# Kernel optimization log

Measured on AMD Instinct MI355X. Metric: run time of the kernel, lower is better.

Reference implementation:

```python
import jax, jax.numpy as jnp
import numpy as np

NS, NV = 32, 8                      # scalar / vector multiplicities
N_NODES, N_EDGES, N_EF = 10000, 100000, 64
W1, W2, W3, W4 = NS*NS, NV*NV, NS*NV, NV*NS   # path weight sizes
WNUM = W1 + W2 + W3 + W4            # 1600
D_NODE = NS + 3*NV                  # 56

def mish(x):
    return x * jnp.tanh(jax.nn.softplus(x))

def setup_inputs() -> dict:
    key = jax.random.key(0)
    ks = jax.random.split(key, 8)
    return dict(
        node_attr=jax.random.normal(ks[0], (N_NODES, D_NODE), jnp.float32),
        edge_index=jax.random.randint(ks[1], (2, N_EDGES), 0, N_NODES),
        edge_attr=jax.random.normal(ks[2], (N_EDGES, N_EF), jnp.float32),
        edge_sh=jax.random.normal(ks[3], (N_EDGES, 4), jnp.float32),
        fc1_w=jax.random.normal(ks[4], (N_EF, N_EF), jnp.float32) / np.sqrt(N_EF),
        fc1_b=jnp.zeros((N_EF,), jnp.float32),
        fc2_w=jax.random.normal(ks[5], (N_EF, WNUM), jnp.float32) / np.sqrt(N_EF),
        fc2_b=jnp.zeros((WNUM,), jnp.float32),
        bn_gamma_s=jnp.ones((NS,), jnp.float32),
        bn_beta_s=jnp.zeros((NS,), jnp.float32),
        bn_gamma_v=jnp.ones((NV,), jnp.float32),
    )

def reference(node_attr, edge_index, edge_attr, edge_sh,
              fc1_w, fc1_b, fc2_w, fc2_b,
              bn_gamma_s, bn_beta_s, bn_gamma_v):
    edge_src, edge_dst = edge_index[0], edge_index[1]
    # edge-conditioned TP weights: Linear -> Mish -> Linear
    w = mish(edge_attr @ fc1_w + fc1_b) @ fc2_w + fc2_b            # [E, WNUM]
    w1 = w[:, :W1].reshape(-1, NS, NS)           # 0e x 0e -> 0e
    w2 = w[:, W1:W1+W2].reshape(-1, NV, NV)      # 1o x 0e -> 1o
    w3 = w[:, W1+W2:W1+W2+W3].reshape(-1, NS, NV)  # 0e x 1o -> 1o
    w4 = w[:, W1+W2+W3:].reshape(-1, NV, NS)     # 1o x 1o -> 0e
    # gather destination node features
    x = node_attr[edge_dst]
    s = x[:, :NS]                                # [E,NS]
    v = x[:, NS:].reshape(-1, NV, 3)             # [E,NV,3]
    sh0 = edge_sh[:, 0]                          # [E]
    sh1 = edge_sh[:, 1:4]                        # [E,3]
    # path normalization: 1/sqrt(total fan-in per output irrep) = 1/sqrt(NS+NV)
    a = 1.0 / np.sqrt(float(NS + NV))
    dot = jnp.einsum('euc,ec->eu', v, sh1) / np.sqrt(3.0)  # CG(1,1,0)
    out_s = a * (jnp.einsum('eu,euw->ew', s * sh0[:, None], w1)
               + jnp.einsum('eu,euw->ew', dot, w4))          # [E,NS]
    out_v = a * (jnp.einsum('euc,euw->ewc', v * sh0[:, None, None], w2)
               + jnp.einsum('eu,ec,euw->ewc', s, sh1, w3))   # [E,NV,3]
    tp = jnp.concatenate([out_s, out_v.reshape(-1, 3*NV)], axis=-1)  # [E,D_NODE]
    # scatter-mean over edge_src
    summ = jax.ops.segment_sum(tp, edge_src, num_segments=N_NODES)
    cnt = jax.ops.segment_sum(jnp.ones((N_EDGES,), tp.dtype), edge_src, num_segments=N_NODES)
    out = summ / jnp.maximum(cnt, 1.0)[:, None]
    # residual (in/out irreps equal -> pad is a no-op)
    out = out + node_attr
    # e3nn-style BatchNorm (training batch stats), eps=1e-4, component norm
    eps = 1e-4
    os = out[:, :NS]
    ov = out[:, NS:].reshape(-1, NV, 3)
    mu = os.mean(axis=0)
    osc = os - mu
    var = (osc * osc).mean(axis=0)
    os_n = osc * jax.lax.rsqrt(var + eps) * bn_gamma_s + bn_beta_s
    vn = (ov * ov).mean(axis=-1).mean(axis=0)                 # [NV]
    ov_n = ov * (jax.lax.rsqrt(vn + eps) * bn_gamma_v)[None, :, None]
    return jnp.concatenate([os_n, ov_n.reshape(-1, 3*NV)], axis=-1)
```

## Files before the change

### kernel.cpp

```cpp
#include <hip/hip_runtime.h>
#include <stdint.h>

#define NNODES 10000
#define NEDGES 100000
#define DNODE 56
#define JTOT 1600
#define EBLK 782
#define TBLK 400

typedef __attribute__((ext_vector_type(8))) short short8;
typedef __attribute__((ext_vector_type(4))) float floatx4;

__device__ __forceinline__ unsigned short f2bf(float f) {
  unsigned u = __float_as_uint(f);
  u = u + 0x7fffu + ((u >> 16) & 1u);
  return (unsigned short)(u >> 16);
}
__device__ __forceinline__ float bf2f(unsigned short u) {
  return __uint_as_float(((unsigned)u) << 16);
}

__device__ __forceinline__ float mishf(float x) {
  float e = __expf(x);
  float z = 1.f + e; z = z * z;
  float t = (z - 1.f) / (z + 1.f);
  t = (x > 40.f) ? 1.f : t;
  return x * t;
}

__device__ __forceinline__ void async_ld16(void* lds, const void* gp) {
  __builtin_amdgcn_global_load_lds(
      (const __attribute__((address_space(1))) unsigned int*)gp,
      (__attribute__((address_space(3))) unsigned int*)lds, 16, 0, 0);
}

__global__ __launch_bounds__(256, 4) void k_hidtr(const float* __restrict__ ea,
                                                  const float* __restrict__ fc1w,
                                                  const float* __restrict__ fc1b,
                                                  const float* __restrict__ fc2w,
                                                  const int* __restrict__ eidx,
                                                  int* __restrict__ cntn,
                                                  unsigned short* __restrict__ hb,
                                                  unsigned short* __restrict__ G) {
  const int bid = blockIdx.x, tid = threadIdx.x;
  if (bid >= EBLK) {
    int idx = (bid - EBLK) * 256 + tid;
    if (idx < 64 * JTOT) {
      int jt = idx >> 10, r = idx & 1023;
      int c = r >> 6, w = r & 63;
      int slot = w >> 3, s = w & 7;
      int g = slot ^ (c & 7);
      int k = g * 8 + s;
      int j = jt * 16 + c;
      G[idx] = f2bf(fc2w[k * JTOT + j]);
    }
    return;
  }
  __shared__ unsigned short T[64 * 72];
  __shared__ unsigned short E[128 * 72];
  __shared__ float b1s[64];
  const int e0 = bid * 128;
  if (tid < 128) {
    int e = e0 + tid;
    if (e < NEDGES) atomicAdd(&cntn[eidx[e]], 1);
  }
  if (tid < 64) b1s[tid] = fc1b[tid];
  #pragma unroll
  for (int it = 0; it < 4; it++) {
    int q = tid + 256 * it;
    int k = q >> 4, j4 = (q & 15) * 4;
    float4 v = *(const float4*)(fc1w + (size_t)q * 4);
    T[(j4+0)*72 + k] = f2bf(v.x);
    T[(j4+1)*72 + k] = f2bf(v.y);
    T[(j4+2)*72 + k] = f2bf(v.z);
    T[(j4+3)*72 + k] = f2bf(v.w);
  }
  #pragma unroll
  for (int it = 0; it < 8; it++) {
    int q = tid + 256 * it;
    int e = q >> 4, k4 = (q & 15) * 4;
    int ge = e0 + e;
    float4 v = (ge < NEDGES) ? *(const float4*)(ea + (size_t)ge * 64 + k4)
                             : make_float4(0.f, 0.f, 0.f, 0.f);
    ushort4 p;
    p.x = f2bf(v.x); p.y = f2bf(v.y); p.z = f2bf(v.z); p.w = f2bf(v.w);
    *(ushort4*)(&E[e*72 + k4]) = p;
  }
  __syncthreads();

  const int wave = tid >> 6, lane = tid & 63, col = lane & 15, rg = lane >> 4;
  short8 bf[2][2];
  #pragma unroll
  for (int nt = 0; nt < 2; nt++) {
    int er = wave*32 + nt*16 + col;
    bf[nt][0] = *(const short8*)(&E[er*72 + rg*8]);
    bf[nt][1] = *(const short8*)(&E[er*72 + 32 + rg*8]);
  }
  floatx4 acc[4][2];
  #pragma unroll
  for (int jt = 0; jt < 4; jt++) {
    int j = jt*16 + col;
    short8 a0 = *(const short8*)(&T[j*72 + rg*8]);
    short8 a1 = *(const short8*)(&T[j*72 + 32 + rg*8]);
    float4 bb = *(const float4*)(&b1s[jt*16 + rg*4]);
    #pragma unroll
    for (int nt = 0; nt < 2; nt++) {
      floatx4 c = {bb.x, bb.y, bb.z, bb.w};
      c = __builtin_amdgcn_mfma_f32_16x16x32_bf16(a0, bf[nt][0], c, 0, 0, 0);
      c = __builtin_amdgcn_mfma_f32_16x16x32_bf16(a1, bf[nt][1], c, 0, 0, 0);
      acc[jt][nt] = c;
    }
  }
  #pragma unroll
  for (int jt = 0; jt < 4; jt++)
    #pragma unroll
    for (int nt = 0; nt < 2; nt++) {
      ushort4 p;
      p.x = f2bf(mishf(acc[jt][nt][0]));
      p.y = f2bf(mishf(acc[jt][nt][1]));
      p.z = f2bf(mishf(acc[jt][nt][2]));
      p.w = f2bf(mishf(acc[jt][nt][3]));
      *(ushort4*)(&E[(wave*32 + nt*16 + col)*72 + jt*16 + rg*4]) = p;
    }
  #pragma unroll
  for (int it = 0; it < 4; it++) {
    int g = it*64 + lane;
    int r = g >> 3, c = g & 7;
    int ge = e0 + wave*32 + r;
    if (ge < NEDGES) {
      short8 v = *(const short8*)(&E[(wave*32 + r)*72 + c*8]);
      *(short8*)(hb + (size_t)ge*64 + c*8) = v;
    }
  }
}

__global__ __launch_bounds__(1024) void k_scan(const int* __restrict__ cntn,
                                               int* __restrict__ offs,
                                               int* __restrict__ cursor) {
  __shared__ int ts[1024];
  int t = threadIdx.x;
  int base = t * 10;
  int loc[10]; int s = 0;
  #pragma unroll
  for (int i = 0; i < 10; i++) {
    int idx = base + i;
    int v = (idx < NNODES) ? cntn[idx] : 0;
    loc[i] = s; s += v;
  }
  ts[t] = s;
  __syncthreads();
  for (int off = 1; off < 1024; off <<= 1) {
    int v = (t >= off) ? ts[t - off] : 0;
    __syncthreads();
    ts[t] += v;
    __syncthreads();
  }
  int excl = (t == 0) ? 0 : ts[t - 1];
  #pragma unroll
  for (int i = 0; i < 10; i++) {
    int idx = base + i;
    if (idx < NNODES) { int o = excl + loc[i]; offs[idx] = o; cursor[idx] = o; }
  }
  if (t == 1023) offs[NNODES] = ts[1023];
}

__global__ __launch_bounds__(256, 4) void k_tp(
    const unsigned short* __restrict__ hb,
    const unsigned short* __restrict__ G,
    const float* __restrict__ fc2b,
    const int* __restrict__ eidx,
    const float* __restrict__ node_attr,
    const float* __restrict__ edge_sh,
    int* __restrict__ cursor,
    float* __restrict__ tp) {
  __shared__ short Gs[2][4 * 1024];
  __shared__ unsigned short wls[4][64 * 32];
  __shared__ float b2s[JTOT];
  __shared__ int pos_s[4][32];
  const int tid = threadIdx.x;
  const int wave = tid >> 6, lane = tid & 63;
  for (int i = tid; i < JTOT; i += 256) b2s[i] = fc2b[i];

  const int e0w = blockIdx.x * 128 + wave * 32;
  unsigned short* Wt = &wls[wave][0];
  {
    int el = lane & 31, hh = lane >> 5;
    int e = e0w + el;
    bool valid = e < NEDGES;
    int dst = valid ? eidx[NEDGES + e] : 0;
    const float* na = node_attr + (size_t)dst * DNODE;
    if (hh == 0) {
      pos_s[wave][el] = valid ? atomicAdd(&cursor[eidx[e]], 1) : 0;
      #pragma unroll
      for (int u = 0; u < 32; u += 4) {
        float4 v = valid ? *(const float4*)(na + u) : make_float4(0.f,0.f,0.f,0.f);
        Wt[(u+0)*32 + el] = f2bf(v.x);
        Wt[(u+1)*32 + el] = f2bf(v.y);
        Wt[(u+2)*32 + el] = f2bf(v.z);
        Wt[(u+3)*32 + el] = f2bf(v.w);
      }
    } else {
      float4 sh = valid ? *(const float4*)(edge_sh + 4*(size_t)e) : make_float4(0.f,0.f,0.f,0.f);
      const float rs3 = 0.57735026918962576f;
      #pragma unroll
      for (int u = 0; u < 8; u++) {
        float v0 = valid ? na[32 + u*3 + 0] : 0.f;
        float v1 = valid ? na[32 + u*3 + 1] : 0.f;
        float v2 = valid ? na[32 + u*3 + 2] : 0.f;
        Wt[(32 + u*3 + 0)*32 + el] = f2bf(v0);
        Wt[(32 + u*3 + 1)*32 + el] = f2bf(v1);
        Wt[(32 + u*3 + 2)*32 + el] = f2bf(v2);
        Wt[(56 + u)*32 + el] = f2bf((v0*sh.y + v1*sh.z + v2*sh.w) * rs3);
      }
    }
  }

  const int col = lane & 15, rg = lane >> 4, rgh = rg >> 1;
  const int g0 = (rg ^ (col & 7)) * 8;
  const int g1 = ((rg + 4) ^ (col & 7)) * 8;
  float sh0c[2], sh1c[2][3];
  bool vld[2];
  short8 bfrag[2][2];
  const short8 zfrag = {0,0,0,0,0,0,0,0};
  #pragma unroll
  for (int nt = 0; nt < 2; nt++) {
    int e = e0w + nt*16 + col;
    bool v = e < NEDGES; vld[nt] = v;
    if (v) {
      float4 sh = *(const float4*)(edge_sh + 4*(size_t)e);
      sh0c[nt] = sh.x; sh1c[nt][0] = sh.y; sh1c[nt][1] = sh.z; sh1c[nt][2] = sh.w;
      const unsigned short* hp = hb + (size_t)e * 64;
      bfrag[nt][0] = *(const short8*)(hp + rg*8);
      bfrag[nt][1] = *(const short8*)(hp + 32 + rg*8);
    } else {
      sh0c[nt] = 0.f; sh1c[nt][0] = sh1c[nt][1] = sh1c[nt][2] = 0.f;
      bfrag[nt][0] = zfrag; bfrag[nt][1] = zfrag;
    }
  }

  float sacc[2][8], vacc[2][12];
  #pragma unroll
  for (int nt = 0; nt < 2; nt++) {
    #pragma unroll
    for (int i = 0; i < 8; i++) sacc[nt][i] = 0.f;
    #pragma unroll
    for (int i = 0; i < 12; i++) vacc[nt][i] = 0.f;
  }

  auto stage = [&](int ch, int b) {
    const unsigned short* gsrc = G + (size_t)ch * 4096 + tid * 8;
    #pragma unroll
    for (int i = 0; i < 2; i++)
      async_ld16(&Gs[b][(i*256 + wave*64) * 8], gsrc + i*256*8);
  };

  const int cc0 = blockIdx.x % 25;
  stage(cc0, 0);
  __syncthreads();

  int buf = 0;
  #pragma unroll 1
  for (int cc = 0; cc < 25; cc++) {
    int c = cc0 + cc; if (c >= 25) c -= 25;
    if (cc < 24) { int cn = c + 1; if (cn >= 25) cn = 0; stage(cn, buf ^ 1); }
    #pragma unroll
    for (int t = 0; t < 4; t++) {
      const int jt = c * 4 + t;
      const short* gb = &Gs[buf][t * 1024];
      short8 x0 = *(const short8*)(gb + col*64 + g0);
      short8 x1 = *(const short8*)(gb + col*64 + g1);
      float4 bb = *(const float4*)&b2s[jt*16 + rg*4];
      floatx4 acc[2];
      #pragma unroll
      for (int nt = 0; nt < 2; nt++) {
        floatx4 a = {bb.x, bb.y, bb.z, bb.w};
        a = __builtin_amdgcn_mfma_f32_16x16x32_bf16(x0, bfrag[nt][0], a, 0, 0, 0);
        a = __builtin_amdgcn_mfma_f32_16x16x32_bf16(x1, bfrag[nt][1], a, 0, 0, 0);
        acc[nt] = a;
      }
      if (jt < 64) {
        const int u = jt >> 1, p = jt & 1;
        #pragma unroll
        for (int nt = 0; nt < 2; nt++) {
          float cf = bf2f(Wt[u*32 + nt*16 + col]) * sh0c[nt];
          #pragma unroll
          for (int r = 0; r < 4; r++)
            sacc[nt][p*4+r] = fmaf(cf, acc[nt][r], sacc[nt][p*4+r]);
        }
      } else if (jt < 68) {
        const int u = (jt - 64)*2 + rgh;
        #pragma unroll
        for (int nt = 0; nt < 2; nt++) {
          #pragma unroll
          for (int q = 0; q < 3; q++) {
            float cf = bf2f(Wt[(32 + u*3 + q)*32 + nt*16 + col]) * sh0c[nt];
            #pragma unroll
            for (int r = 0; r < 4; r++)
              vacc[nt][q*4+r] = fmaf(cf, acc[nt][r], vacc[nt][q*4+r]);
          }
        }
      } else if (jt < 84) {
        const int u = (jt - 68)*2 + rgh;
        #pragma unroll
        for (int nt = 0; nt < 2; nt++) {
          float sv = bf2f(Wt[u*32 + nt*16 + col]);
          #pragma unroll
          for (int q = 0; q < 3; q++) {
            float cf = sv * sh1c[nt][q];
            #pragma unroll
            for (int r = 0; r < 4; r++)
              vacc[nt][q*4+r] = fmaf(cf, acc[nt][r], vacc[nt][q*4+r]);
          }
        }
      } else {
        const int u = (jt - 84) >> 1, p = jt & 1;
        #pragma unroll
        for (int nt = 0; nt < 2; nt++) {
          float cf = bf2f(Wt[(56 + u)*32 + nt*16 + col]);
          #pragma unroll
          for (int r = 0; r < 4; r++)
            sacc[nt][p*4+r] = fmaf(cf, acc[nt][r], sacc[nt][p*4+r]);
        }
      }
    }
    buf ^= 1;
    __syncthreads();
  }

  const float ascale = 0.15811388300841897f;
  #pragma unroll
  for (int nt = 0; nt < 2; nt++) {
    int el = nt*16 + col;
    float* rowp = tp + (size_t)pos_s[wave][el] * DNODE;
    if (vld[nt]) {
      #pragma unroll
      for (int p = 0; p < 2; p++) {
        float4 v = make_float4(ascale*sacc[nt][p*4+0], ascale*sacc[nt][p*4+1],
                               ascale*sacc[nt][p*4+2], ascale*sacc[nt][p*4+3]);
        *(float4*)(rowp + p*16 + rg*4) = v;
      }
    }
    float vtot[12];
    #pragma unroll
    for (int k = 0; k < 12; k++)
      vtot[k] = (vacc[nt][k] + __shfl_xor(vacc[nt][k], 32)) * ascale;
    if (rg < 2 && vld[nt]) {
      float tmp[12];
      #pragma unroll
      for (int q = 0; q < 3; q++)
        #pragma unroll
        for (int r = 0; r < 4; r++) tmp[r*3 + q] = vtot[q*4 + r];
      #pragma unroll
      for (int j = 0; j < 3; j++)
        *(float4*)(rowp + 32 + (rg & 1)*12 + j*4) = *(float4*)&tmp[j*4];
    }
  }
}

__global__ __launch_bounds__(256) void k_gather(const float* __restrict__ tp,
                                                const int* __restrict__ offs,
                                                const float* __restrict__ node_attr,
                                                float* __restrict__ pre,
                                                float* __restrict__ pstat) {
  __shared__ float redS[4*64], redQ[4*64];
  int t = threadIdx.x, wave = t >> 6, lane = t & 63;
  int gw = blockIdx.x * 4 + wave;
  const int W = 640 * 4;
  int off = (lane < DNODE) ? lane : 0;
  float ssum = 0.f, ssq = 0.f;
  for (int n = gw; n < NNODES; n += W) {
    int beg = offs[n], end = offs[n+1];
    float acc = 0.f;
    int i = beg;
    for (; i + 4 <= end; i += 4) {
      float v0 = tp[(size_t)(i+0)*DNODE + off];
      float v1 = tp[(size_t)(i+1)*DNODE + off];
      float v2 = tp[(size_t)(i+2)*DNODE + off];
      float v3 = tp[(size_t)(i+3)*DNODE + off];
      acc += (v0 + v1) + (v2 + v3);
    }
    for (; i < end; i++) acc += tp[(size_t)i*DNODE + off];
    int c = end - beg; if (c < 1) c = 1;
    float m = acc / (float)c + node_attr[(size_t)n*DNODE + off];
    if (lane < DNODE) { pre[(size_t)n*DNODE + lane] = m; ssum += m; ssq += m*m; }
  }
  redS[wave*64 + lane] = ssum;
  redQ[wave*64 + lane] = ssq;
  __syncthreads();
  if (wave == 0 && lane < DNODE) {
    float a = redS[lane] + redS[64+lane] + redS[128+lane] + redS[192+lane];
    float b = redQ[lane] + redQ[64+lane] + redQ[128+lane] + redQ[192+lane];
    pstat[(size_t)blockIdx.x*112 + lane] = a;
    pstat[(size_t)blockIdx.x*112 + 56 + lane] = b;
  }
}

__global__ __launch_bounds__(256) void k_stats(const float* __restrict__ pstat,
                                               float* __restrict__ stats) {
  int f = blockIdx.x * 4 + (threadIdx.x >> 6);
  int lane = threadIdx.x & 63;
  float v = 0.f;
  for (int b = lane; b < 640; b += 64) v += pstat[(size_t)b*112 + f];
  #pragma unroll
  for (int o = 32; o; o >>= 1) v += __shfl_xor(v, o);
  if (lane == 0) stats[f] = v;
}

__global__ __launch_bounds__(256) void k_norm(const float* __restrict__ pre,
                                              const float* __restrict__ stats,
                                              const float* __restrict__ gs,
                                              const float* __restrict__ bs,
                                              const float* __restrict__ gv,
                                              float* __restrict__ out) {
  int idx = blockIdx.x * 256 + threadIdx.x;
  if (idx >= NNODES * DNODE) return;
  int n = idx / DNODE;
  int d = idx - n * DNODE;
  float val = pre[idx];
  const float invN = 1.f / (float)NNODES;
  float res;
  if (d < 32) {
    float mu = stats[d] * invN;
    float var = stats[56 + d] * invN - mu * mu;
    res = (val - mu) * rsqrtf(var + 1e-4f) * gs[d] + bs[d];
  } else {
    int wi = (d - 32) / 3;
    float vn = (stats[56 + 32 + wi*3] + stats[56 + 32 + wi*3 + 1] +
                stats[56 + 32 + wi*3 + 2]) * (invN / 3.f);
    res = val * rsqrtf(vn + 1e-4f) * gv[wi];
  }
  out[idx] = res;
}

extern "C" void kernel_launch(void* const* d_in, const int* in_sizes, int n_in,
                              void* d_out, int out_size, void* d_ws, size_t ws_size,
                              hipStream_t stream) {
  const float* node_attr = (const float*)d_in[0];
  const int*   eidx      = (const int*)d_in[1];
  const float* edge_attr = (const float*)d_in[2];
  const float* edge_sh   = (const float*)d_in[3];
  const float* fc1w      = (const float*)d_in[4];
  const float* fc1b      = (const float*)d_in[5];
  const float* fc2w      = (const float*)d_in[6];
  const float* fc2b      = (const float*)d_in[7];
  const float* gs        = (const float*)d_in[8];
  const float* bs        = (const float*)d_in[9];
  const float* gv        = (const float*)d_in[10];

  float* ws = (float*)d_ws;
  float* tp    = ws;
  float* pre   = ws + 5600000;
  float* stats = ws + 6160000;
  float* pstat = ws + 6160128;
  int*   cntn  = (int*)(ws + 6231808);
  int*   offs  = (int*)(ws + 6241808);
  int*   cursor= (int*)(ws + 6251816);
  unsigned short* G  = (unsigned short*)(ws + 6261816);
  unsigned short* hb = (unsigned short*)(ws + 6313016);

  hipMemsetAsync(cntn, 0, (size_t)10000 * 4, stream);
  k_hidtr<<<EBLK + TBLK, 256, 0, stream>>>(edge_attr, fc1w, fc1b, fc2w, eidx, cntn, hb, G);
  k_scan<<<1, 1024, 0, stream>>>(cntn, offs, cursor);
  k_tp<<<782, 256, 0, stream>>>(hb, G, fc2b, eidx, node_attr, edge_sh, cursor, tp);
  k_gather<<<640, 256, 0, stream>>>(tp, offs, node_attr, pre, pstat);
  k_stats<<<28, 256, 0, stream>>>(pstat, stats);
  k_norm<<<(NNODES * DNODE + 255) / 256, 256, 0, stream>>>(pre, stats, gs, bs, gv, (float*)d_out);
}
```

Before: 195.9 us.

## Switch TP GEMM to 32x32 MFMA tiles and fuse scan/stats into neighbors

The edge tensor-product kernel now uses 32x32x16 bf16 MFMA tiles, one 32-edge column per wave, with a re-laid-out fc2 weight matrix. This removes the cross-half shuffle reduction and lowers instruction count per output. Separately, the histogram and scan are done by one extra block inside the hidden-layer kernel, which eliminates the memset and the scan launch. The stats reduction is folded into the gather kernel through a last-block atomic counter, which removes another launch. The costs are a serial single-block histogram of 100k edges and higher LDS use, with occupancy dropped to 3 blocks.

After: 312.1 us. 59.3% more time.

```diff
diff --git a/kernel.cpp b/kernel.cpp
--- a/kernel.cpp
+++ b/kernel.cpp
@@ -9,7 +9,7 @@
 #define TBLK 400
 
 typedef __attribute__((ext_vector_type(8))) short short8;
-typedef __attribute__((ext_vector_type(4))) float floatx4;
+typedef __attribute__((ext_vector_type(16))) float floatx16;
 
 __device__ __forceinline__ unsigned short f2bf(float f) {
   unsigned u = __float_as_uint(f);
@@ -34,36 +34,69 @@
       (__attribute__((address_space(3))) unsigned int*)lds, 16, 0, 0);
 }
 
-__global__ __launch_bounds__(256, 4) void k_hidtr(const float* __restrict__ ea,
+__global__ __launch_bounds__(256, 3) void k_hidtr(const float* __restrict__ ea,
                                                   const float* __restrict__ fc1w,
                                                   const float* __restrict__ fc1b,
                                                   const float* __restrict__ fc2w,
                                                   const int* __restrict__ eidx,
-                                                  int* __restrict__ cntn,
+                                                  int* __restrict__ offs,
+                                                  int* __restrict__ cursor,
+                                                  int* __restrict__ gdone,
                                                   unsigned short* __restrict__ hb,
                                                   unsigned short* __restrict__ G) {
+  __shared__ int4 SM4[2576];
   const int bid = blockIdx.x, tid = threadIdx.x;
+
+  if (bid == EBLK + TBLK) {
+    int* hist = (int*)SM4;
+    int* ts   = hist + 10000;
+    for (int i = tid; i < NNODES; i += 256) hist[i] = 0;
+    if (tid == 0) gdone[0] = 0;
+    __syncthreads();
+    for (int i = tid; i < NEDGES; i += 256) atomicAdd(&hist[eidx[i]], 1);
+    __syncthreads();
+    int s = 0;
+    #pragma unroll 8
+    for (int i = 0; i < 40; i++) {
+      int idx = tid * 40 + i;
+      if (idx < NNODES) s += hist[idx];
+    }
+    ts[tid] = s;
+    __syncthreads();
+    for (int o = 1; o < 256; o <<= 1) {
+      int v = (tid >= o) ? ts[tid - o] : 0;
+      __syncthreads();
+      ts[tid] += v;
+      __syncthreads();
+    }
+    int run = (tid == 0) ? 0 : ts[tid - 1];
+    for (int i = 0; i < 40; i++) {
+      int idx = tid * 40 + i;
+      if (idx < NNODES) { int c = hist[idx]; offs[idx] = run; cursor[idx] = run; run += c; }
+    }
+    if (tid == 255) offs[NNODES] = ts[255];
+    return;
+  }
+
   if (bid >= EBLK) {
     int idx = (bid - EBLK) * 256 + tid;
     if (idx < 64 * JTOT) {
-      int jt = idx >> 10, r = idx & 1023;
-      int c = r >> 6, w = r & 63;
-      int slot = w >> 3, s = w & 7;
-      int g = slot ^ (c & 7);
-      int k = g * 8 + s;
-      int j = jt * 16 + c;
+      int jt = idx >> 11;
+      int r  = idx & 2047;
+      int s  = r >> 9;
+      int l  = (r >> 3) & 63;
+      int i  = r & 7;
+      int j  = jt * 32 + (l & 31);
+      int k  = s * 16 + (l >> 5) * 8 + i;
       G[idx] = f2bf(fc2w[k * JTOT + j]);
     }
     return;
   }
-  __shared__ unsigned short T[64 * 72];
-  __shared__ unsigned short E[128 * 72];
-  __shared__ float b1s[64];
+
+  unsigned short* T  = (unsigned short*)SM4;
+  unsigned short* E  = (unsigned short*)SM4 + 4608;
+  float* b1s = (float*)((char*)SM4 + 27648);
   const int e0 = bid * 128;
-  if (tid < 128) {
-    int e = e0 + tid;
-    if (e < NEDGES) atomicAdd(&cntn[eidx[e]], 1);
-  }
   if (tid < 64) b1s[tid] = fc1b[tid];
   #pragma unroll
   for (int it = 0; it < 4; it++) {
@@ -89,6 +122,7 @@
   __syncthreads();
 
   const int wave = tid >> 6, lane = tid & 63, col = lane & 15, rg = lane >> 4;
+  typedef __attribute__((ext_vector_type(4))) float floatx4;
   short8 bf[2][2];
   #pragma unroll
   for (int nt = 0; nt < 2; nt++) {
@@ -132,36 +166,6 @@
       *(short8*)(hb + (size_t)ge*64 + c*8) = v;
     }
   }
-}
-
-__global__ __launch_bounds__(1024) void k_scan(const int* __restrict__ cntn,
-                                               int* __restrict__ offs,
-                                               int* __restrict__ cursor) {
-  __shared__ int ts[1024];
-  int t = threadIdx.x;
-  int base = t * 10;
-  int loc[10]; int s = 0;
-  #pragma unroll
-  for (int i = 0; i < 10; i++) {
-    int idx = base + i;
-    int v = (idx < NNODES) ? cntn[idx] : 0;
-    loc[i] = s; s += v;
-  }
-  ts[t] = s;
-  __syncthreads();
-  for (int off = 1; off < 1024; off <<= 1) {
-    int v = (t >= off) ? ts[t - off] : 0;
-    __syncthreads();
-    ts[t] += v;
-    __syncthreads();
-  }
-  int excl = (t == 0) ? 0 : ts[t - 1];
-  #pragma unroll
-  for (int i = 0; i < 10; i++) {
-    int idx = base + i;
-    if (idx < NNODES) { int o = excl + loc[i]; offs[idx] = o; cursor[idx] = o; }
-  }
-  if (t == 1023) offs[NNODES] = ts[1023];
 }
 
 __global__ __launch_bounds__(256, 4) void k_tp(
@@ -173,8 +177,8 @@
     const float* __restrict__ edge_sh,
     int* __restrict__ cursor,
     float* __restrict__ tp) {
-  __shared__ short Gs[2][4 * 1024];
-  __shared__ unsigned short wls[4][64 * 32];
+  __shared__ short Gs[2][4096];
+  __shared__ unsigned short wls[4][2048];
   __shared__ float b2s[JTOT];
   __shared__ int pos_s[4][32];
   const int tid = threadIdx.x;
@@ -215,37 +219,30 @@
     }
   }
 
-  const int col = lane & 15, rg = lane >> 4, rgh = rg >> 1;
-  const int g0 = (rg ^ (col & 7)) * 8;
-  const int g1 = ((rg + 4) ^ (col & 7)) * 8;
-  float sh0c[2], sh1c[2][3];
-  bool vld[2];
-  short8 bfrag[2][2];
+  const int col = lane & 31, h = lane >> 5;
+  const int e = e0w + col;
+  const bool vld = e < NEDGES;
+  float sh0c, sh1c[3];
+  short8 bfr[4];
   const short8 zfrag = {0,0,0,0,0,0,0,0};
-  #pragma unroll
-  for (int nt = 0; nt < 2; nt++) {
-    int e = e0w + nt*16 + col;
-    bool v = e < NEDGES; vld[nt] = v;
-    if (v) {
-      float4 sh = *(const float4*)(edge_sh + 4*(size_t)e);
-      sh0c[nt] = sh.x; sh1c[nt][0] = sh.y; sh1c[nt][1] = sh.z; sh1c[nt][2] = sh.w;
-      const unsigned short* hp = hb + (size_t)e * 64;
-      bfrag[nt][0] = *(const short8*)(hp + rg*8);
-      bfrag[nt][1] = *(const short8*)(hp + 32 + rg*8);
-    } else {
-      sh0c[nt] = 0.f; sh1c[nt][0] = sh1c[nt][1] = sh1c[nt][2] = 0.f;
-      bfrag[nt][0] = zfrag; bfrag[nt][1] = zfrag;
-    }
-  }
-
-  float sacc[2][8], vacc[2][12];
-  #pragma unroll
-  for (int nt = 0; nt < 2; nt++) {
-    #pragma unroll
-    for (int i = 0; i < 8; i++) sacc[nt][i] = 0.f;
-    #pragma unroll
-    for (int i = 0; i < 12; i++) vacc[nt][i] = 0.f;
-  }
+  if (vld) {
+    float4 sh = *(const float4*)(edge_sh + 4*(size_t)e);
+    sh0c = sh.x; sh1c[0] = sh.y; sh1c[1] = sh.z; sh1c[2] = sh.w;
+    const unsigned short* hp = hb + (size_t)e * 64;
+    #pragma unroll
+    for (int s = 0; s < 4; s++)
+      bfr[s] = *(const short8*)(hp + s*16 + h*8);
+  } else {
+    sh0c = 0.f; sh1c[0] = sh1c[1] = sh1c[2] = 0.f;
+    #pragma unroll
+    for (int s = 0; s < 4; s++) bfr[s] = zfrag;
+  }
+
+  float sacc[16], vacc[12];
+  #pragma unroll
+  for (int i = 0; i < 16; i++) sacc[i] = 0.f;
+  #pragma unroll
+  for (int i = 0; i < 12; i++) vacc[i] = 0.f;
 
   auto stage = [&](int ch, int b) {
     const unsigned short* gsrc = G + (size_t)ch * 4096 + tid * 8;
@@ -254,106 +251,107 @@
       async_ld16(&Gs[b][(i*256 + wave*64) * 8], gsrc + i*256*8);
   };
 
+  int buf = 0;
+  auto gemm_tile = [&](int jt, int t) -> floatx16 {
+    const short* gb = &Gs[buf][t * 2048];
+    short8 a0 = *(const short8*)(gb + lane*8);
+    short8 a1 = *(const short8*)(gb + 512 + lane*8);
+    short8 a2 = *(const short8*)(gb + 1024 + lane*8);
+    short8 a3 = *(const short8*)(gb + 1536 + lane*8);
+    floatx16 C;
+    #pragma unroll
+    for (int q = 0; q < 4; q++) {
+      float4 b = *(const float4*)&b2s[jt*32 + 8*q + 4*h];
+      C[q*4+0] = b.x; C[q*4+1] = b.y; C[q*4+2] = b.z; C[q*4+3] = b.w;
+    }
+    C = __builtin_amdgcn_mfma_f32_32x32x16_bf16(a0, bfr[0], C, 0, 0, 0);
+    C = __builtin_amdgcn_mfma_f32_32x32x16_bf16(a1, bfr[1], C, 0, 0, 0);
+    C = __builtin_amdgcn_mfma_f32_32x32x16_bf16(a2, bfr[2], C, 0, 0, 0);
+    C = __builtin_amdgcn_mfma_f32_32x32x16_bf16(a3, bfr[3], C, 0, 0, 0);
+    return C;
+  };
+  auto apply_s = [&](const floatx16& C, float cf) {
+    #pragma unroll
+    for (int i = 0; i < 16; i++) sacc[i] = fmaf(cf, C[i], sacc[i]);
+  };
+  auto apply_w2 = [&](const floatx16& C, int ubase) {
+    #pragma unroll
+    for (int q = 0; q < 4; q++) {
+      const int u = ubase + q;
+      #pragma unroll
+      for (int c = 0; c < 3; c++) {
+        float cf = bf2f(Wt[(32 + u*3 + c)*32 + col]) * sh0c;
+        #pragma unroll
+        for (int r = 0; r < 4; r++)
+          vacc[c*4+r] = fmaf(cf, C[q*4+r], vacc[c*4+r]);
+      }
+    }
+  };
+  auto apply_w3 = [&](const floatx16& C, int ubase) {
+    #pragma unroll
+    for (int q = 0; q < 4; q++) {
+      float sv = bf2f(Wt[(ubase + q)*32 + col]);
+      #pragma unroll
+      for (int c = 0; c < 3; c++) {
+        float cf = sv * sh1c[c];
+        #pragma unroll
+        for (int r = 0; r < 4; r++)
+          vacc[c*4+r] = fmaf(cf, C[q*4+r], vacc[c*4+r]);
+      }
+    }
+  };
+
   const int cc0 = blockIdx.x % 25;
   stage(cc0, 0);
   __syncthreads();
 
-  int buf = 0;
   #pragma unroll 1
   for (int cc = 0; cc < 25; cc++) {
     int c = cc0 + cc; if (c >= 25) c -= 25;
     if (cc < 24) { int cn = c + 1; if (cn >= 25) cn = 0; stage(cn, buf ^ 1); }
-    #pragma unroll
-    for (int t = 0; t < 4; t++) {
-      const int jt = c * 4 + t;
-      const short* gb = &Gs[buf][t * 1024];
-      short8 x0 = *(const short8*)(gb + col*64 + g0);
-      short8 x1 = *(const short8*)(gb + col*64 + g1);
-      float4 bb = *(const float4*)&b2s[jt*16 + rg*4];
-      floatx4 acc[2];
-      #pragma unroll
-      for (int nt = 0; nt < 2; nt++) {
-        floatx4 a = {bb.x, bb.y, bb.z, bb.w};
-        a = __builtin_amdgcn_mfma_f32_16x16x32_bf16(x0, bfrag[nt][0], a, 0, 0, 0);
-        a = __builtin_amdgcn_mfma_f32_16x16x32_bf16(x1, bfrag[nt][1], a, 0, 0, 0);
-        acc[nt] = a;
-      }
-      if (jt < 64) {
-        const int u = jt >> 1, p = jt & 1;
-        #pragma unroll
-        for (int nt = 0; nt < 2; nt++) {
-          float cf = bf2f(Wt[u*32 + nt*16 + col]) * sh0c[nt];
-          #pragma unroll
-          for (int r = 0; r < 4; r++)
-            sacc[nt][p*4+r] = fmaf(cf, acc[nt][r], sacc[nt][p*4+r]);
-        }
-      } else if (jt < 68) {
-        const int u = (jt - 64)*2 + rgh;
-        #pragma unroll
-        for (int nt = 0; nt < 2; nt++) {
-          #pragma unroll
-          for (int q = 0; q < 3; q++) {
-            float cf = bf2f(Wt[(32 + u*3 + q)*32 + nt*16 + col]) * sh0c[nt];
-            #pragma unroll
-            for (int r = 0; r < 4; r++)
-              vacc[nt][q*4+r] = fmaf(cf, acc[nt][r], vacc[nt][q*4+r]);
-          }
-        }
-      } else if (jt < 84) {
-        const int u = (jt - 68)*2 + rgh;
-        #pragma unroll
-        for (int nt = 0; nt < 2; nt++) {
-          float sv = bf2f(Wt[u*32 + nt*16 + col]);
-          #pragma unroll
-          for (int q = 0; q < 3; q++) {
-            float cf = sv * sh1c[nt][q];
-            #pragma unroll
-            for (int r = 0; r < 4; r++)
-              vacc[nt][q*4+r] = fmaf(cf, acc[nt][r], vacc[nt][q*4+r]);
-          }
-        }
-      } else {
-        const int u = (jt - 84) >> 1, p = jt & 1;
-        #pragma unroll
-        for (int nt = 0; nt < 2; nt++) {
-          float cf = bf2f(Wt[(56 + u)*32 + nt*16 + col]);
-          #pragma unroll
-          for (int r = 0; r < 4; r++)
-            sacc[nt][p*4+r] = fmaf(cf, acc[nt][r], sacc[nt][p*4+r]);
-        }
-      }
+    const int jt0 = c * 2;
+    if (jt0 < 32) {
+      floatx16 C0 = gemm_tile(jt0, 0);
+      apply_s(C0, bf2f(Wt[jt0*32 + col]) * sh0c);
+      floatx16 C1 = gemm_tile(jt0 + 1, 1);
+      apply_s(C1, bf2f(Wt[(jt0+1)*32 + col]) * sh0c);
+    } else if (jt0 == 32) {
+      floatx16 C0 = gemm_tile(32, 0);
+      apply_w2(C0, 0);
+      floatx16 C1 = gemm_tile(33, 1);
+      apply_w2(C1, 4);
+    } else if (jt0 < 42) {
+      floatx16 C0 = gemm_tile(jt0, 0);
+      apply_w3(C0, (jt0 - 34) * 4);
+      floatx16 C1 = gemm_tile(jt0 + 1, 1);
+      apply_w3(C1, (jt0 - 33) * 4);
+    } else {
+      floatx16 C0 = gemm_tile(jt0, 0);
+      apply_s(C0, bf2f(Wt[(56 + jt0 - 42)*32 + col]));
+      floatx16 C1 = gemm_tile(jt0 + 1, 1);
+      apply_s(C1, bf2f(Wt[(56 + jt0 - 41)*32 + col]));
     }
     buf ^= 1;
     __syncthreads();
   }
 
   const float ascale = 0.15811388300841897f;
-  #pragma unroll
-  for (int nt = 0; nt < 2; nt++) {
-    int el = nt*16 + col;
-    float* rowp = tp + (size_t)pos_s[wave][el] * DNODE;
-    if (vld[nt]) {
+  if (vld) {
+    float* rowp = tp + (size_t)pos_s[wave][col] * DNODE;
+    #pragma unroll
+    for (int q = 0; q < 4; q++) {
+      float4 v = make_float4(ascale*sacc[q*4+0], ascale*sacc[q*4+1],
+                             ascale*sacc[q*4+2], ascale*sacc[q*4+3]);
+      *(float4*)(rowp + 8*q + 4*h) = v;
+    }
+    float tmp[12];
+    #pragma unroll
+    for (int r = 0; r < 4; r++)
       #pragma unroll
-      for (int p = 0; p < 2; p++) {
-        float4 v = make_float4(ascale*sacc[nt][p*4+0], ascale*sacc[nt][p*4+1],
-                               ascale*sacc[nt][p*4+2], ascale*sacc[nt][p*4+3]);
-        *(float4*)(rowp + p*16 + rg*4) = v;
-      }
-    }
-    float vtot[12];
-    #pragma unroll
-    for (int k = 0; k < 12; k++)
-      vtot[k] = (vacc[nt][k] + __shfl_xor(vacc[nt][k], 32)) * ascale;
-    if (rg < 2 && vld[nt]) {
-      float tmp[12];
-      #pragma unroll
-      for (int q = 0; q < 3; q++)
-        #pragma unroll
-        for (int r = 0; r < 4; r++) tmp[r*3 + q] = vtot[q*4 + r];
-      #pragma unroll
-      for (int j = 0; j < 3; j++)
-        *(float4*)(rowp + 32 + (rg & 1)*12 + j*4) = *(float4*)&tmp[j*4];
-    }
+      for (int c = 0; c < 3; c++) tmp[r*3 + c] = ascale * vacc[c*4 + r];
+    #pragma unroll
+    for (int j = 0; j < 3; j++)
+      *(float4*)(rowp + 32 + 12*h + j*4) = *(float4*)&tmp[j*4];
   }
 }
 
@@ -361,8 +359,11 @@
                                                 const int* __restrict__ offs,
                                                 const float* __restrict__ node_attr,
                                                 float* __restrict__ pre,
-                                                float* __restrict__ pstat) {
+                                                float* __restrict__ pstat,
+                                                int* __restrict__ gdone,
+                                                float* __restrict__ stats) {
   __shared__ float redS[4*64], redQ[4*64];
+  __shared__ int amLast;
   int t = threadIdx.x, wave = t >> 6, lane = t & 63;
   int gw = blockIdx.x * 4 + wave;
   const int W = 640 * 4;
@@ -393,17 +394,24 @@
     pstat[(size_t)blockIdx.x*112 + lane] = a;
     pstat[(size_t)blockIdx.x*112 + 56 + lane] = b;
   }
-}
-
-__global__ __launch_bounds__(256) void k_stats(const float* __restrict__ pstat,
-                                               float* __restrict__ stats) {
-  int f = blockIdx.x * 4 + (threadIdx.x >> 6);
-  int lane = threadIdx.x & 63;
-  float v = 0.f;
-  for (int b = lane; b < 640; b += 64) v += pstat[(size_t)b*112 + f];
-  #pragma unroll
-  for (int o = 32; o; o >>= 1) v += __shfl_xor(v, o);
-  if (lane == 0) stats[f] = v;
+  __syncthreads();
+  if (t == 0) {
+    __threadfence();
+    amLast = (atomicAdd(gdone, 1) == 639) ? 1 : 0;
+  }
+  __syncthreads();
+  if (amLast) {
+    __threadfence();
+    int f = t & 127, hh = t >> 7;
+    float v = 0.f;
+    if (f < 112) {
+      #pragma unroll 8
+      for (int b = hh; b < 640; b += 2) v += pstat[(size_t)b*112 + f];
+      redS[hh*128 + f] = v;
+    }
+    __syncthreads();
+    if (t < 112) stats[t] = redS[t] + redS[128 + t];
+  }
 }
 
 __global__ __launch_bounds__(256) void k_norm(const float* __restrict__ pre,
@@ -452,17 +460,15 @@
   float* pre   = ws + 5600000;
   float* stats = ws + 6160000;
   float* pstat = ws + 6160128;
-  int*   cntn  = (int*)(ws + 6231808);
-  int*   offs  = (int*)(ws + 6241808);
-  int*   cursor= (int*)(ws + 6251816);
-  unsigned short* G  = (unsigned short*)(ws + 6261816);
-  unsigned short* hb = (unsigned short*)(ws + 6313016);
-
-  hipMemsetAsync(cntn, 0, (size_t)10000 * 4, stream);
-  k_hidtr<<<EBLK + TBLK, 256, 0, stream>>>(edge_attr, fc1w, fc1b, fc2w, eidx, cntn, hb, G);
-  k_scan<<<1, 1024, 0, stream>>>(cntn, offs, cursor);
+  int*   offs  = (int*)(ws + 6231808);
+  int*   cursor= (int*)(ws + 6241816);
+  int*   gdone = (int*)(ws + 6251816);
+  unsigned short* G  = (unsigned short*)(ws + 6251824);
+  unsigned short* hb = (unsigned short*)(ws + 6303024);
+
+  k_hidtr<<<EBLK + TBLK + 1, 256, 0, stream>>>(edge_attr, fc1w, fc1b, fc2w, eidx,
+                                               offs, cursor, gdone, hb, G);
   k_tp<<<782, 256, 0, stream>>>(hb, G, fc2b, eidx, node_attr, edge_sh, cursor, tp);
-  k_gather<<<640, 256, 0, stream>>>(tp, offs, node_attr, pre, pstat);
-  k_stats<<<28, 256, 0, stream>>>(pstat, stats);
+  k_gather<<<640, 256, 0, stream>>>(tp, offs, node_attr, pre, pstat, gdone, stats);
   k_norm<<<(NNODES * DNODE + 255) / 256, 256, 0, stream>>>(pre, stats, gs, bs, gv, (float*)d_out);
 }
```
